# Kernel optimization log

Hardware: AMD Instinct MI355X
Metric: run time of the kernel (lower is better)

Reference implementation:

```python
import jax, jax.numpy as jnp
import numpy as np

N_NODES = 100000
N_EDGES = 1600000
H_DIM = 64  # pos(32) + vel(32)


def _mlp_init(key, d_in, d_hid, d_out):
    k1, k2 = jax.random.split(key)
    s1 = 1.0 / np.sqrt(d_in)
    s2 = 1.0 / np.sqrt(d_hid)
    w1 = jax.random.uniform(k1, (d_in, d_hid), jnp.float32, -s1, s1)
    w2 = jax.random.uniform(k2, (d_hid, d_out), jnp.float32, -s2, s2)
    return w1, jnp.zeros((d_hid,), jnp.float32), w2, jnp.zeros((d_out,), jnp.float32)


def setup_inputs() -> dict:
    key = jax.random.key(0)
    ks = jax.random.split(key, 6)
    pos = jax.random.normal(ks[0], (N_NODES, 32), jnp.float32)
    vel = jax.random.normal(ks[1], (N_NODES, 32), jnp.float32)
    edge_index = jax.random.randint(ks[2], (2, N_EDGES), 0, N_NODES, jnp.int32)
    msg_w1, msg_b1, msg_w2, msg_b2 = _mlp_init(ks[3], 2 * H_DIM, 64, 64)
    upd_w1, upd_b1, upd_w2, upd_b2 = _mlp_init(ks[4], H_DIM + 64, 64, 64)
    sp = 1.0 / np.sqrt(64)
    pred_w = jax.random.uniform(ks[5], (64, 32), jnp.float32, -sp, sp)
    pred_b = jnp.zeros((32,), jnp.float32)
    return dict(pos=pos, vel=vel, edge_index=edge_index,
                msg_w1=msg_w1, msg_b1=msg_b1, msg_w2=msg_w2, msg_b2=msg_b2,
                upd_w1=upd_w1, upd_b1=upd_b1, upd_w2=upd_w2, upd_b2=upd_b2,
                pred_w=pred_w, pred_b=pred_b)


def reference(pos, vel, edge_index,
              msg_w1, msg_b1, msg_w2, msg_b2,
              upd_w1, upd_b1, upd_w2, upd_b2,
              pred_w, pred_b):
    n = pos.shape[0]
    h = jnp.concatenate([pos, vel], axis=-1)              # [N, 64]
    src, dst = edge_index[0], edge_index[1]
    h_i = h[dst]                                          # [E, 64] target nodes
    h_j = h[src]                                          # [E, 64] source nodes
    # message MLP on concat(h_i, h_j)
    m = jnp.concatenate([h_i, h_j], axis=-1)              # [E, 128]
    m = jax.nn.relu(m @ msg_w1 + msg_b1) @ msg_w2 + msg_b2  # [E, 64]
    # scatter-add aggregate to target nodes
    aggr = jax.ops.segment_sum(m, dst, num_segments=n)    # [N, 64]
    # update MLP on concat(h, aggr)
    u = jnp.concatenate([h, aggr], axis=-1)               # [N, 128]
    u = jax.nn.relu(u @ upd_w1 + upd_b1) @ upd_w2 + upd_b2  # [N, 64]
    # linear prediction head -> acceleration
    return u @ pred_w + pred_b                            # [N, 32]
```

## Files before the change

kernel.cpp:

```cpp
#include <hip/hip_runtime.h>

#define NN 100000
#define NE 1600000
#define SB   391
#define NBKT 391
#define EPB  4096

typedef _Float16 f16x8 __attribute__((ext_vector_type(8)));
typedef float    f32x4 __attribute__((ext_vector_type(4)));

#define ZB   1563
#define PHB  3125
#define PWB  13

extern "C" __global__ void __launch_bounds__(256)
prep_kernel(const float* __restrict__ pos, const float* __restrict__ vel,
            const float* __restrict__ mw1, const float* __restrict__ mw2,
            const float* __restrict__ uw1, const float* __restrict__ uw2,
            const float* __restrict__ pw,
            _Float16* __restrict__ hh,
            _Float16* __restrict__ mw1f, _Float16* __restrict__ mw2f,
            _Float16* __restrict__ uw1f, _Float16* __restrict__ uw2f,
            _Float16* __restrict__ pwf,
            float* __restrict__ aggr)
{
    const int b = blockIdx.x, tid = threadIdx.x;
    if (b < ZB) {
        float4* p = (float4*)aggr;
        const int base4 = b * 1024 + tid;
        const float4 z = make_float4(0.f, 0.f, 0.f, 0.f);
#pragma unroll
        for (int k = 0; k < 4; ++k) {
            const int idx = base4 + k * 256;
            if (idx < NN * 16) p[idx] = z;
        }
    } else if (b < ZB + PHB) {
        const int t = (b - ZB) * 256 + tid;
        const int node = t >> 3, seg = t & 7;
        const float* src = (seg < 4) ? pos + (size_t)node * 32 + seg * 8
                                     : vel + (size_t)node * 32 + (seg - 4) * 8;
        const float4 a = ((const float4*)src)[0];
        const float4 c = ((const float4*)src)[1];
        f16x8 r;
        r[0]=(_Float16)a.x; r[1]=(_Float16)a.y; r[2]=(_Float16)a.z; r[3]=(_Float16)a.w;
        r[4]=(_Float16)c.x; r[5]=(_Float16)c.y; r[6]=(_Float16)c.z; r[7]=(_Float16)c.w;
        *(f16x8*)(hh + (size_t)node * 64 + seg * 8) = r;
    } else {
        const int t2 = (b - ZB - PHB) * 256 + tid;
        if (t2 < 1024) {
            const int t = t2 >> 8, kk = (t2 >> 6) & 3, l = t2 & 63;
            f16x8 r;
#pragma unroll
            for (int j = 0; j < 8; ++j)
                r[j] = (_Float16)mw1[(kk * 32 + (l >> 4) * 8 + j) * 64 + t * 16 + (l & 15)];
            *(f16x8*)(mw1f + (size_t)t2 * 8) = r;
        } else if (t2 < 1536) {
            const int i = t2 - 1024;
            const int t = i >> 7, kk = (i >> 6) & 1, l = i & 63;
            f16x8 r;
#pragma unroll
            for (int j = 0; j < 8; ++j)
                r[j] = (_Float16)mw2[(kk * 32 + (l >> 4) * 8 + j) * 64 + t * 16 + (l & 15)];
            *(f16x8*)(mw2f + (size_t)i * 8) = r;
        } else if (t2 < 2560) {
            const int i = t2 - 1536;
            const int t = i >> 8, kk = (i >> 6) & 3, l = i & 63;
            f16x8 r;
#pragma unroll
            for (int j = 0; j < 8; ++j)
                r[j] = (_Float16)uw1[(kk * 32 + (l >> 4) * 8 + j) * 64 + t * 16 + (l & 15)];
            *(f16x8*)(uw1f + (size_t)i * 8) = r;
        } else if (t2 < 3072) {
            const int i = t2 - 2560;
            const int t = i >> 7, kk = (i >> 6) & 1, l = i & 63;
            f16x8 r;
#pragma unroll
            for (int j = 0; j < 8; ++j)
                r[j] = (_Float16)uw2[(kk * 32 + (l >> 4) * 8 + j) * 64 + t * 16 + (l & 15)];
            *(f16x8*)(uw2f + (size_t)i * 8) = r;
        } else if (t2 < 3328) {
            const int i = t2 - 3072;
            const int t = i >> 7, kk = (i >> 6) & 1, l = i & 63;
            f16x8 r;
#pragma unroll
            for (int j = 0; j < 8; ++j)
                r[j] = (_Float16)pw[(kk * 32 + (l >> 4) * 8 + j) * 32 + t * 16 + (l & 15)];
            *(f16x8*)(pwf + (size_t)i * 8) = r;
        }
    }
}

extern "C" __global__ void __launch_bounds__(256)
sortA_kernel(const int* __restrict__ ei, int* __restrict__ cntm)
{
    __shared__ int lh[NBKT];
    const int tid = threadIdx.x, blk = blockIdx.x;
    for (int i = tid; i < NBKT; i += 256) lh[i] = 0;
    __syncthreads();
    const int e0 = blk * EPB;
#pragma unroll
    for (int k = 0; k < EPB / 256; ++k) {
        const int e = e0 + k * 256 + tid;
        if (e < NE) atomicAdd(&lh[ei[NE + e] >> 8], 1);
    }
    __syncthreads();
    for (int i = tid; i < NBKT; i += 256) cntm[blk * NBKT + i] = lh[i];
}

extern "C" __global__ void __launch_bounds__(512)
scancol_kernel(const int* __restrict__ cntm, int* __restrict__ offs,
               int* __restrict__ btot)
{
    __shared__ int s[512];
    const int tid = threadIdx.x, bkt = blockIdx.x;
    const int v = (tid < SB) ? cntm[tid * NBKT + bkt] : 0;
    s[tid] = v;
    __syncthreads();
    for (int off = 1; off < 512; off <<= 1) {
        int t = (tid >= off) ? s[tid - off] : 0;
        __syncthreads();
        s[tid] += t;
        __syncthreads();
    }
    if (tid < SB) offs[tid * NBKT + bkt] = s[tid] - v;
    if (tid == SB - 1) btot[bkt] = s[tid];
}

extern "C" __global__ void __launch_bounds__(512)
scanb_kernel(const int* __restrict__ btot, int* __restrict__ bbase)
{
    __shared__ int s[512];
    const int tid = threadIdx.x;
    const int v = (tid < NBKT) ? btot[tid] : 0;
    s[tid] = v;
    __syncthreads();
    for (int off = 1; off < 512; off <<= 1) {
        int t = (tid >= off) ? s[tid - off] : 0;
        __syncthreads();
        s[tid] += t;
        __syncthreads();
    }
    if (tid < NBKT) bbase[tid] = s[tid] - v;
    if (tid == NBKT - 1) bbase[NBKT] = s[tid];
}

extern "C" __global__ void __launch_bounds__(256)
sortC_kernel(const int* __restrict__ ei, const int* __restrict__ offs,
             const int* __restrict__ bbase, int2* __restrict__ sd_tmp)
{
    __shared__ int lh[NBKT];
    __shared__ int lo[NBKT];
    const int tid = threadIdx.x, blk = blockIdx.x;
    for (int i = tid; i < NBKT; i += 256) {
        lh[i] = 0;
        lo[i] = bbase[i] + offs[blk * NBKT + i];
    }
    __syncthreads();
    const int e0 = blk * EPB;
#pragma unroll
    for (int k = 0; k < EPB / 256; ++k) {
        const int e = e0 + k * 256 + tid;
        if (e < NE) {
            const int s = ei[e], d = ei[NE + e];
            const int bkt = d >> 8;
            const int r = atomicAdd(&lh[bkt], 1);
            sd_tmp[lo[bkt] + r] = make_int2(s, d);
        }
    }
}

extern "C" __global__ void __launch_bounds__(256)
sortD_kernel(const int2* __restrict__ sd_tmp, const int* __restrict__ bbase,
             int2* __restrict__ sd2)
{
    __shared__ int h[256];
    __shared__ int s[256];
    __shared__ int dbase[256];
    const int tid = threadIdx.x, bkt = blockIdx.x;
    const int s0 = bbase[bkt], s1 = bbase[bkt + 1];
    const int n = s1 - s0;
    h[tid] = 0;
    __syncthreads();
    for (int k = tid; k < n; k += 256)
        atomicAdd(&h[sd_tmp[s0 + k].y & 255], 1);
    __syncthreads();
    const int v = h[tid];
    s[tid] = v;
    __syncthreads();
    for (int off = 1; off < 256; off <<= 1) {
        int t = (tid >= off) ? s[tid - off] : 0;
        __syncthreads();
        s[tid] += t;
        __syncthreads();
    }
    dbase[tid] = s[tid] - v;
    __syncthreads();
    h[tid] = 0;
    __syncthreads();
    for (int k = tid; k < n; k += 256) {
        const int2 e = sd_tmp[s0 + k];
        const int dl = e.y & 255;
        const int r = atomicAdd(&h[dl], 1);
        sd2[s0 + dbase[dl] + r] = e;
    }
}

extern "C" __global__ void __launch_bounds__(256)
edgeagg_kernel(const _Float16* __restrict__ hh,
               const int2* __restrict__ sd,
               const _Float16* __restrict__ w1f, const _Float16* __restrict__ w2f,
               const float* __restrict__ b1, const float* __restrict__ b2,
               float* __restrict__ aggr)
{
    __shared__ _Float16 sW1[4 * 4 * 64 * 8];
    __shared__ _Float16 sW2[4 * 2 * 64 * 8];
    __shared__ _Float16 sT[4][16 * 64];

    const int tid = threadIdx.x;
    const int wave = tid >> 6, lane = tid & 63;
    const int m = lane & 15, g = lane >> 4;
    const int wslot = (blockIdx.x * 4 + wave) * 64;

    const int2 sdv = sd[wslot + lane];

    const int prevd = __shfl_up(sdv.y, 1, 64);
    const unsigned long long bmask = __ballot(lane == 0 || sdv.y != prevd);

    {
        const uint4* g1 = (const uint4*)w1f; uint4* s1 = (uint4*)sW1;
#pragma unroll
        for (int i = 0; i < 4; ++i) s1[i * 256 + tid] = g1[i * 256 + tid];
        const uint4* g2 = (const uint4*)w2f; uint4* s2 = (uint4*)sW2;
#pragma unroll
        for (int i = 0; i < 2; ++i) s2[i * 256 + tid] = g2[i * 256 + tid];
    }

    const float bb1[4] = { b1[m], b1[16 + m], b1[32 + m], b1[48 + m] };
    const float bb2[4] = { b2[m], b2[16 + m], b2[32 + m], b2[48 + m] };

    __syncthreads();

    _Float16* Y = sT[wave];

    float racc = 0.0f;
    int   rnode = __builtin_amdgcn_readlane(sdv.y, 0);
    int   firstRun = 1;

    f16x8 Abuf[2][4];
    {
        const int ns = __shfl(sdv.x, m, 64);
        const int nd = __shfl(sdv.y, m, 64);
        const _Float16* hd = hh + (size_t)nd * 64 + g * 8;
        const _Float16* hs = hh + (size_t)ns * 64 + g * 8;
        Abuf[0][0] = *(const f16x8*)(hd);
        Abuf[0][1] = *(const f16x8*)(hd + 32);
        Abuf[0][2] = *(const f16x8*)(hs);
        Abuf[0][3] = *(const f16x8*)(hs + 32);
    }

#pragma unroll
    for (int it = 0; it < 4; ++it) {
        const int cur = it & 1;
        if (it < 3) {
            const int ns = __shfl(sdv.x, (it + 1) * 16 + m, 64);
            const int nd = __shfl(sdv.y, (it + 1) * 16 + m, 64);
            const _Float16* hd = hh + (size_t)nd * 64 + g * 8;
            const _Float16* hs = hh + (size_t)ns * 64 + g * 8;
            Abuf[cur ^ 1][0] = *(const f16x8*)(hd);
            Abuf[cur ^ 1][1] = *(const f16x8*)(hd + 32);
            Abuf[cur ^ 1][2] = *(const f16x8*)(hs);
            Abuf[cur ^ 1][3] = *(const f16x8*)(hs + 32);
        }

        f32x4 acc[4] = {};
#pragma unroll
        for (int t = 0; t < 4; ++t) {
#pragma unroll
            for (int kk = 0; kk < 4; ++kk) {
                const f16x8 b = *(const f16x8*)(sW1 + ((t * 4 + kk) * 64 + lane) * 8);
                acc[t] = __builtin_amdgcn_mfma_f32_16x16x32_f16(Abuf[cur][kk], b, acc[t], 0, 0, 0);
            }
        }

#pragma unroll
        for (int t = 0; t < 4; ++t) {
#pragma unroll
            for (int r = 0; r < 4; ++r) {
                const float y = fmaxf(acc[t][r] + bb1[t], 0.0f);
                const int row = g * 4 + r, col = t * 16 + m;
                const int byteoff = row * 128 + ((2 * col) ^ ((row & 7) << 4));
                *(_Float16*)((char*)Y + byteoff) = (_Float16)y;
            }
        }
        asm volatile("s_waitcnt lgkmcnt(0)" ::: "memory");
        __builtin_amdgcn_sched_barrier(0);

        f16x8 a2[2];
#pragma unroll
        for (int kk = 0; kk < 2; ++kk) {
            const int c = kk * 4 + g;
            a2[kk] = *(const f16x8*)((char*)Y + m * 128 + ((c * 16) ^ ((m & 7) << 4)));
        }
        asm volatile("s_waitcnt lgkmcnt(0)" ::: "memory");
        __builtin_amdgcn_sched_barrier(0);

        f32x4 acc2[4] = {};
#pragma unroll
        for (int kk = 0; kk < 2; ++kk) {
#pragma unroll
            for (int t = 0; t < 4; ++t) {
                const f16x8 b = *(const f16x8*)(sW2 + ((t * 2 + kk) * 64 + lane) * 8);
                acc2[t] = __builtin_amdgcn_mfma_f32_16x16x32_f16(a2[kk], b, acc2[t], 0, 0, 0);
            }
        }
#pragma unroll
        for (int t = 0; t < 4; ++t)
#pragma unroll
            for (int r = 0; r < 4; ++r) acc2[t][r] += bb2[t];

        const unsigned tm = (unsigned)((bmask >> (it * 16)) & 0xFFFFull) | 0x10000u;
        int a = 0;
        while (a < 16) {
            const int b = a + 1 + __builtin_ctz(tm >> (a + 1));
            const int d = __builtin_amdgcn_readlane(sdv.y, it * 16 + a);
            if (d != rnode) {
                float* ap = aggr + (size_t)rnode * 64 + lane;
                if (firstRun) atomicAdd(ap, racc);
                else          *ap = racc;
                firstRun = 0; racc = 0.0f; rnode = d;
            }
            float p0 = 0.f, p1 = 0.f, p2 = 0.f, p3 = 0.f;
#pragma unroll
            for (int r = 0; r < 4; ++r) {
                const int rowl = 4 * g + r;
                const bool in = (rowl >= a) && (rowl < b);
                p0 += in ? acc2[0][r] : 0.f;
                p1 += in ? acc2[1][r] : 0.f;
                p2 += in ? acc2[2][r] : 0.f;
                p3 += in ? acc2[3][r] : 0.f;
            }
            p0 += __shfl_xor(p0, 16); p0 += __shfl_xor(p0, 32);
            p1 += __shfl_xor(p1, 16); p1 += __shfl_xor(p1, 32);
            p2 += __shfl_xor(p2, 16); p2 += __shfl_xor(p2, 32);
            p3 += __shfl_xor(p3, 16); p3 += __shfl_xor(p3, 32);
            const float v = (g == 0) ? p0 : (g == 1) ? p1 : (g == 2) ? p2 : p3;
            racc += v;
            a = b;
        }
    }
    atomicAdd(aggr + (size_t)rnode * 64 + lane, racc);
}

extern "C" __global__ void __launch_bounds__(256)
node_mfma_kernel(const _Float16* __restrict__ hh, const float* __restrict__ aggr,
                 const _Float16* __restrict__ uw1f, const _Float16* __restrict__ uw2f,
                 const _Float16* __restrict__ pwf,
                 const float* __restrict__ b1, const float* __restrict__ b2,
                 const float* __restrict__ pb, float* __restrict__ out)
{
    __shared__ _Float16 sU1[4 * 4 * 64 * 8];
    __shared__ _Float16 sU2[4 * 2 * 64 * 8];
    __shared__ _Float16 sPW[2 * 2 * 64 * 8];
    __shared__ _Float16 sT[4][16 * 64];

    const int tid = threadIdx.x;
    {
        const uint4* g1 = (const uint4*)uw1f; uint4* s1 = (uint4*)sU1;
#pragma unroll
        for (int i = 0; i < 4; ++i) s1[i * 256 + tid] = g1[i * 256 + tid];
        const uint4* g2 = (const uint4*)uw2f; uint4* s2 = (uint4*)sU2;
#pragma unroll
        for (int i = 0; i < 2; ++i) s2[i * 256 + tid] = g2[i * 256 + tid];
        const uint4* g3 = (const uint4*)pwf;  uint4* s3 = (uint4*)sPW;
        s3[tid] = g3[tid];
    }
    __syncthreads();

    const int wave = tid >> 6, lane = tid & 63;
    const int m = lane & 15, g = lane >> 4;
    const int nb = (blockIdx.x * 4 + wave) * 16;
    const int v = nb + m;
    const int vl = (v < NN) ? v : (NN - 1);

    const _Float16* hv = hh + (size_t)vl * 64 + g * 8;
    const f16x8 a0 = *(const f16x8*)(hv);
    const f16x8 a1 = *(const f16x8*)(hv + 32);
    const float* av = aggr + (size_t)vl * 64 + g * 8;
    const float4 x0 = *(const float4*)(av),      x1 = *(const float4*)(av + 4);
    const float4 y0 = *(const float4*)(av + 32), y1 = *(const float4*)(av + 36);
    f16x8 a2, a3;
    a2[0]=(_Float16)x0.x; a2[1]=(_Float16)x0.y; a2[2]=(_Float16)x0.z; a2[3]=(_Float16)x0.w;
    a2[4]=(_Float16)x1.x; a2[5]=(_Float16)x1.y; a2[6]=(_Float16)x1.z; a2[7]=(_Float16)x1.w;
    a3[0]=(_Float16)y0.x; a3[1]=(_Float16)y0.y; a3[2]=(_Float16)y0.z; a3[3]=(_Float16)y0.w;
    a3[4]=(_Float16)y1.x; a3[5]=(_Float16)y1.y; a3[6]=(_Float16)y1.z; a3[7]=(_Float16)y1.w;

    f32x4 acc[4] = {};
#pragma unroll
    for (int t = 0; t < 4; ++t) {
        acc[t] = __builtin_amdgcn_mfma_f32_16x16x32_f16(
            a0, *(const f16x8*)(sU1 + ((t * 4 + 0) * 64 + lane) * 8), acc[t], 0, 0, 0);
        acc[t] = __builtin_amdgcn_mfma_f32_16x16x32_f16(
            a1, *(const f16x8*)(sU1 + ((t * 4 + 1) * 64 + lane) * 8), acc[t], 0, 0, 0);
        acc[t] = __builtin_amdgcn_mfma_f32_16x16x32_f16(
            a2, *(const f16x8*)(sU1 + ((t * 4 + 2) * 64 + lane) * 8), acc[t], 0, 0, 0);
        acc[t] = __builtin_amdgcn_mfma_f32_16x16x32_f16(
            a3, *(const f16x8*)(sU1 + ((t * 4 + 3) * 64 + lane) * 8), acc[t], 0, 0, 0);
    }

    _Float16* Y = sT[wave];
#pragma unroll
    for (int t = 0; t < 4; ++t) {
        const float bb = b1[t * 16 + m];
#pragma unroll
        for (int r = 0; r < 4; ++r) {
            const float y = fmaxf(acc[t][r] + bb, 0.0f);
            const int row = g * 4 + r, col = t * 16 + m;
            const int byteoff = row * 128 + ((2 * col) ^ ((row & 7) << 4));
            *(_Float16*)((char*)Y + byteoff) = (_Float16)y;
        }
    }
    asm volatile("s_waitcnt lgkmcnt(0)" ::: "memory");
    __builtin_amdgcn_sched_barrier(0);

    f16x8 ay[2];
#pragma unroll
    for (int kk = 0; kk < 2; ++kk) {
        const int c = kk * 4 + g;
        ay[kk] = *(const f16x8*)((char*)Y + m * 128 + ((c * 16) ^ ((m & 7) << 4)));
    }
    asm volatile("s_waitcnt lgkmcnt(0)" ::: "memory");
    __builtin_amdgcn_sched_barrier(0);

    f32x4 acc2[4] = {};
#pragma unroll
    for (int kk = 0; kk < 2; ++kk) {
#pragma unroll
        for (int t = 0; t < 4; ++t) {
            const f16x8 b = *(const f16x8*)(sU2 + ((t * 2 + kk) * 64 + lane) * 8);
            acc2[t] = __builtin_amdgcn_mfma_f32_16x16x32_f16(ay[kk], b, acc2[t], 0, 0, 0);
        }
    }

#pragma unroll
    for (int t = 0; t < 4; ++t) {
        const float bb = b2[t * 16 + m];
#pragma unroll
        for (int r = 0; r < 4; ++r) {
            const float u = acc2[t][r] + bb;
            const int row = g * 4 + r, col = t * 16 + m;
            const int byteoff = row * 128 + ((2 * col) ^ ((row & 7) << 4));
            *(_Float16*)((char*)Y + byteoff) = (_Float16)u;
        }
    }
    asm volatile("s_waitcnt lgkmcnt(0)" ::: "memory");
    __builtin_amdgcn_sched_barrier(0);

    f16x8 au[2];
#pragma unroll
    for (int kk = 0; kk < 2; ++kk) {
        const int c = kk * 4 + g;
        au[kk] = *(const f16x8*)((char*)Y + m * 128 + ((c * 16) ^ ((m & 7) << 4)));
    }
    asm volatile("s_waitcnt lgkmcnt(0)" ::: "memory");
    __builtin_amdgcn_sched_barrier(0);

    f32x4 acc3[2] = {};
#pragma unroll
    for (int kk = 0; kk < 2; ++kk) {
#pragma unroll
        for (int t = 0; t < 2; ++t) {
            const f16x8 b = *(const f16x8*)(sPW + ((t * 2 + kk) * 64 + lane) * 8);
            acc3[t] = __builtin_amdgcn_mfma_f32_16x16x32_f16(au[kk], b, acc3[t], 0, 0, 0);
        }
    }

    float* F = (float*)Y;
#pragma unroll
    for (int t = 0; t < 2; ++t) {
        const float bb = pb[t * 16 + m];
#pragma unroll
        for (int r = 0; r < 4; ++r) {
            const int row = g * 4 + r, col = t * 16 + m;
            const int byteoff = row * 128 + ((4 * col) ^ ((row & 7) << 4));
            *(float*)((char*)F + byteoff) = acc3[t][r] + bb;
        }
    }
    asm volatile("s_waitcnt lgkmcnt(0)" ::: "memory");
    __builtin_amdgcn_sched_barrier(0);

    const int row = lane >> 2, q = lane & 3;
    const float4 o0 = *(const float4*)((char*)F + row * 128 + ((q * 16)       ^ ((row & 7) << 4)));
    const float4 o1 = *(const float4*)((char*)F + row * 128 + (((q + 4) * 16) ^ ((row & 7) << 4)));
    if (nb + row < NN) {
        float4* op = (float4*)(out + (size_t)(nb + row) * 32);
        op[q]     = o0;
        op[q + 4] = o1;
    }
}

extern "C" __global__ void __launch_bounds__(256)
edge_msg_kernel(const float* __restrict__ pos, const float* __restrict__ vel,
                const int* __restrict__ ei,
                const float* __restrict__ w1, const float* __restrict__ b1,
                const float* __restrict__ w2, const float* __restrict__ b2,
                float* __restrict__ aggr)
{
    const int e = blockIdx.x * 256 + threadIdx.x;
    if (e >= NE) return;
    const int ns = ei[e];
    const int nd = ei[NE + e];
    float y[64];
#pragma unroll
    for (int j = 0; j < 64; ++j) y[j] = b1[j];
    for (int part = 0; part < 4; ++part) {
        const int    node  = (part < 2) ? nd : ns;
        const float* basep = (part & 1) ? vel : pos;
        const float4* xp = reinterpret_cast<const float4*>(basep + (size_t)node * 32);
        const float*  wp = w1 + part * 32 * 64;
        for (int q = 0; q < 8; ++q) {
            const float4 xv = xp[q];
#pragma unroll
            for (int kk = 0; kk < 4; ++kk) {
                const float xs = (kk == 0) ? xv.x : (kk == 1) ? xv.y
                               : (kk == 2) ? xv.z : xv.w;
                const float* wr = wp + (q * 4 + kk) * 64;
#pragma unroll
                for (int j = 0; j < 64; ++j) y[j] = fmaf(xs, wr[j], y[j]);
            }
        }
    }
    float mm[64];
#pragma unroll
    for (int c = 0; c < 64; ++c) mm[c] = b2[c];
#pragma unroll
    for (int j = 0; j < 64; ++j) {
        const float yj = fmaxf(y[j], 0.0f);
        const float* wr = w2 + j * 64;
#pragma unroll
        for (int c = 0; c < 64; ++c) mm[c] = fmaf(yj, wr[c], mm[c]);
    }
    float* ap = aggr + (size_t)nd * 64;
#pragma unroll
    for (int c = 0; c < 64; ++c) atomicAdd(ap + c, mm[c]);
}

extern "C" __global__ void __launch_bounds__(256)
node_upd_kernel(const float* __restrict__ pos, const float* __restrict__ vel,
                const float* __restrict__ aggr,
                const float* __restrict__ w1, const float* __restrict__ b1,
                const float* __restrict__ w2, const float* __restrict__ b2,
                const float* __restrict__ pw, const float* __restrict__ pb,
                float* __restrict__ out)
{
    const int v = blockIdx.x * 256 + threadIdx.x;
    if (v >= NN) return;

    float y[64];
#pragma unroll
    for (int j = 0; j < 64; ++j) y[j] = b1[j];
    for (int part = 0; part < 4; ++part) {
        const float* basep = (part == 0) ? pos + (size_t)v * 32
                           : (part == 1) ? vel + (size_t)v * 32
                           : aggr + (size_t)v * 64 + (size_t)(part - 2) * 32;
        const float4* xp = reinterpret_cast<const float4*>(basep);
        const float*  wp = w1 + part * 32 * 64;
        for (int q = 0; q < 8; ++q) {
            const float4 xv = xp[q];
#pragma unroll
            for (int kk = 0; kk < 4; ++kk) {
                const float xs = (kk == 0) ? xv.x : (kk == 1) ? xv.y
                               : (kk == 2) ? xv.z : xv.w;
                const float* wr = wp + (q * 4 + kk) * 64;
#pragma unroll
                for (int j = 0; j < 64; ++j) y[j] = fmaf(xs, wr[j], y[j]);
            }
        }
    }

    float u[64];
#pragma unroll
    for (int c = 0; c < 64; ++c) u[c] = b2[c];
#pragma unroll
    for (int j = 0; j < 64; ++j) {
        const float yj = fmaxf(y[j], 0.0f);
        const float* wr = w2 + j * 64;
#pragma unroll
        for (int c = 0; c < 64; ++c) u[c] = fmaf(yj, wr[c], u[c]);
    }

    float o[32];
#pragma unroll
    for (int c = 0; c < 32; ++c) o[c] = pb[c];
#pragma unroll
    for (int j = 0; j < 64; ++j) {
        const float* wr = pw + j * 32;
#pragma unroll
        for (int c = 0; c < 32; ++c) o[c] = fmaf(u[j], wr[c], o[c]);
    }

    float4* op = reinterpret_cast<float4*>(out + (size_t)v * 32);
#pragma unroll
    for (int q = 0; q < 8; ++q)
        op[q] = make_float4(o[q * 4], o[q * 4 + 1], o[q * 4 + 2], o[q * 4 + 3]);
}

extern "C" void kernel_launch(void* const* d_in, const int* in_sizes, int n_in,
                              void* d_out, int out_size, void* d_ws, size_t ws_size,
                              hipStream_t stream)
{
    const float* pos = (const float*)d_in[0];
    const float* vel = (const float*)d_in[1];
    const int*   ei  = (const int*)d_in[2];
    const float* mw1 = (const float*)d_in[3];
    const float* mb1 = (const float*)d_in[4];
    const float* mw2 = (const float*)d_in[5];
    const float* mb2 = (const float*)d_in[6];
    const float* uw1 = (const float*)d_in[7];
    const float* ub1 = (const float*)d_in[8];
    const float* uw2 = (const float*)d_in[9];
    const float* ub2 = (const float*)d_in[10];
    const float* pw  = (const float*)d_in[11];
    const float* pb  = (const float*)d_in[12];
    float* out = (float*)d_out;

    char* ws = (char*)d_ws;
    size_t off = 0;
    float*    aggr   = (float*)(ws + off);    off += (size_t)NN * 64 * 4;
    _Float16* hh     = (_Float16*)(ws + off); off += (size_t)NN * 64 * 2;
    int2*     sd_tmp = (int2*)(ws + off);     off += (size_t)NE * 8;
    int2*     sd2    = (int2*)(ws + off);     off += (size_t)NE * 8;
    int*      cntm   = (int*)(ws + off);      off += (size_t)SB * NBKT * 4;
    int*      offs   = (int*)(ws + off);      off += (size_t)SB * NBKT * 4;
    int*      btot   = (int*)(ws + off);      off += 512 * 4;
    int*      bbase  = (int*)(ws + off);      off += 512 * 4;
    _Float16* mw1f   = (_Float16*)(ws + off); off += 1024 * 8 * 2;
    _Float16* mw2f   = (_Float16*)(ws + off); off += 512 * 8 * 2;
    _Float16* uw1f   = (_Float16*)(ws + off); off += 1024 * 8 * 2;
    _Float16* uw2f   = (_Float16*)(ws + off); off += 512 * 8 * 2;
    _Float16* pwf    = (_Float16*)(ws + off); off += 256 * 8 * 2;
    const size_t need_full = off;

    if (ws_size >= need_full) {
        prep_kernel<<<ZB + PHB + PWB, 256, 0, stream>>>(
            pos, vel, mw1, mw2, uw1, uw2, pw,
            hh, mw1f, mw2f, uw1f, uw2f, pwf, aggr);
        sortA_kernel<<<SB, 256, 0, stream>>>(ei, cntm);
        scancol_kernel<<<NBKT, 512, 0, stream>>>(cntm, offs, btot);
        scanb_kernel<<<1, 512, 0, stream>>>(btot, bbase);
        sortC_kernel<<<SB, 256, 0, stream>>>(ei, offs, bbase, sd_tmp);
        sortD_kernel<<<NBKT, 256, 0, stream>>>(sd_tmp, bbase, sd2);
        edgeagg_kernel<<<NE / 256, 256, 0, stream>>>(
            hh, sd2, mw1f, mw2f, mb1, mb2, aggr);
        node_mfma_kernel<<<(NN + 63) / 64, 256, 0, stream>>>(
            hh, aggr, uw1f, uw2f, pwf, ub1, ub2, pb, out);
    } else {
        float* aggr2 = (float*)d_ws;
        hipMemsetAsync(aggr2, 0, (size_t)NN * 64 * sizeof(float), stream);
        edge_msg_kernel<<<NE / 256, 256, 0, stream>>>(pos, vel, ei,
                                                      mw1, mb1, mw2, mb2, aggr2);
        node_upd_kernel<<<(NN + 255) / 256, 256, 0, stream>>>(
            pos, vel, aggr2, uw1, ub1, uw2, ub2, pw, pb, out);
    }
}
```

Baseline: 138.7 us.

## Fuse sort histogram into prep kernel, widen edge blocks, add fast no-boundary path

```diff
diff --git a/kernel.cpp b/kernel.cpp
--- a/kernel.cpp
+++ b/kernel.cpp
@@ -15,6 +15,7 @@
 
 extern "C" __global__ void __launch_bounds__(256)
 prep_kernel(const float* __restrict__ pos, const float* __restrict__ vel,
+            const int* __restrict__ ei,
             const float* __restrict__ mw1, const float* __restrict__ mw2,
             const float* __restrict__ uw1, const float* __restrict__ uw2,
             const float* __restrict__ pw,
@@ -22,8 +23,9 @@
             _Float16* __restrict__ mw1f, _Float16* __restrict__ mw2f,
             _Float16* __restrict__ uw1f, _Float16* __restrict__ uw2f,
             _Float16* __restrict__ pwf,
-            float* __restrict__ aggr)
-{
+            float* __restrict__ aggr, int* __restrict__ cntm)
+{
+    __shared__ int lh[NBKT];
     const int b = blockIdx.x, tid = threadIdx.x;
     if (b < ZB) {
         float4* p = (float4*)aggr;
@@ -45,7 +47,7 @@
         r[0]=(_Float16)a.x; r[1]=(_Float16)a.y; r[2]=(_Float16)a.z; r[3]=(_Float16)a.w;
         r[4]=(_Float16)c.x; r[5]=(_Float16)c.y; r[6]=(_Float16)c.z; r[7]=(_Float16)c.w;
         *(f16x8*)(hh + (size_t)node * 64 + seg * 8) = r;
-    } else {
+    } else if (b < ZB + PHB + PWB) {
         const int t2 = (b - ZB - PHB) * 256 + tid;
         if (t2 < 1024) {
             const int t = t2 >> 8, kk = (t2 >> 6) & 3, l = t2 & 63;
@@ -87,24 +89,19 @@
                 r[j] = (_Float16)pw[(kk * 32 + (l >> 4) * 8 + j) * 32 + t * 16 + (l & 15)];
             *(f16x8*)(pwf + (size_t)i * 8) = r;
         }
-    }
-}
-
-extern "C" __global__ void __launch_bounds__(256)
-sortA_kernel(const int* __restrict__ ei, int* __restrict__ cntm)
-{
-    __shared__ int lh[NBKT];
-    const int tid = threadIdx.x, blk = blockIdx.x;
-    for (int i = tid; i < NBKT; i += 256) lh[i] = 0;
-    __syncthreads();
-    const int e0 = blk * EPB;
-#pragma unroll
-    for (int k = 0; k < EPB / 256; ++k) {
-        const int e = e0 + k * 256 + tid;
-        if (e < NE) atomicAdd(&lh[ei[NE + e] >> 8], 1);
-    }
-    __syncthreads();
-    for (int i = tid; i < NBKT; i += 256) cntm[blk * NBKT + i] = lh[i];
+    } else {
+        const int blk = b - (ZB + PHB + PWB);
+        for (int i = tid; i < NBKT; i += 256) lh[i] = 0;
+        __syncthreads();
+        const int e0 = blk * EPB;
+#pragma unroll
+        for (int k = 0; k < EPB / 256; ++k) {
+            const int e = e0 + k * 256 + tid;
+            if (e < NE) atomicAdd(&lh[ei[NE + e] >> 8], 1);
+        }
+        __syncthreads();
+        for (int i = tid; i < NBKT; i += 256) cntm[blk * NBKT + i] = lh[i];
+    }
 }
 
 extern "C" __global__ void __launch_bounds__(512)
@@ -205,7 +202,7 @@
     }
 }
 
-extern "C" __global__ void __launch_bounds__(256)
+extern "C" __global__ void __launch_bounds__(512, 8)
 edgeagg_kernel(const _Float16* __restrict__ hh,
                const int2* __restrict__ sd,
                const _Float16* __restrict__ w1f, const _Float16* __restrict__ w2f,
@@ -214,12 +211,12 @@
 {
     __shared__ _Float16 sW1[4 * 4 * 64 * 8];
     __shared__ _Float16 sW2[4 * 2 * 64 * 8];
-    __shared__ _Float16 sT[4][16 * 64];
+    __shared__ _Float16 sT[8][16 * 64];
 
     const int tid = threadIdx.x;
     const int wave = tid >> 6, lane = tid & 63;
     const int m = lane & 15, g = lane >> 4;
-    const int wslot = (blockIdx.x * 4 + wave) * 64;
+    const int wslot = (blockIdx.x * 8 + wave) * 64;
 
     const int2 sdv = sd[wslot + lane];
 
@@ -229,10 +226,9 @@
     {
         const uint4* g1 = (const uint4*)w1f; uint4* s1 = (uint4*)sW1;
 #pragma unroll
-        for (int i = 0; i < 4; ++i) s1[i * 256 + tid] = g1[i * 256 + tid];
+        for (int i = 0; i < 2; ++i) s1[i * 512 + tid] = g1[i * 512 + tid];
         const uint4* g2 = (const uint4*)w2f; uint4* s2 = (uint4*)sW2;
-#pragma unroll
-        for (int i = 0; i < 2; ++i) s2[i * 256 + tid] = g2[i * 256 + tid];
+        s2[tid] = g2[tid];
     }
 
     const float bb1[4] = { b1[m], b1[16 + m], b1[32 + m], b1[48 + m] };
@@ -319,33 +315,46 @@
             for (int r = 0; r < 4; ++r) acc2[t][r] += bb2[t];
 
         const unsigned tm = (unsigned)((bmask >> (it * 16)) & 0xFFFFull) | 0x10000u;
-        int a = 0;
-        while (a < 16) {
-            const int b = a + 1 + __builtin_ctz(tm >> (a + 1));
-            const int d = __builtin_amdgcn_readlane(sdv.y, it * 16 + a);
-            if (d != rnode) {
-                float* ap = aggr + (size_t)rnode * 64 + lane;
-                if (firstRun) atomicAdd(ap, racc);
-                else          *ap = racc;
-                firstRun = 0; racc = 0.0f; rnode = d;
-            }
+        if (tm == 0x10000u) {
             float p0 = 0.f, p1 = 0.f, p2 = 0.f, p3 = 0.f;
 #pragma unroll
             for (int r = 0; r < 4; ++r) {
-                const int rowl = 4 * g + r;
-                const bool in = (rowl >= a) && (rowl < b);
-                p0 += in ? acc2[0][r] : 0.f;
-                p1 += in ? acc2[1][r] : 0.f;
-                p2 += in ? acc2[2][r] : 0.f;
-                p3 += in ? acc2[3][r] : 0.f;
+                p0 += acc2[0][r]; p1 += acc2[1][r];
+                p2 += acc2[2][r]; p3 += acc2[3][r];
             }
             p0 += __shfl_xor(p0, 16); p0 += __shfl_xor(p0, 32);
             p1 += __shfl_xor(p1, 16); p1 += __shfl_xor(p1, 32);
             p2 += __shfl_xor(p2, 16); p2 += __shfl_xor(p2, 32);
             p3 += __shfl_xor(p3, 16); p3 += __shfl_xor(p3, 32);
-            const float v = (g == 0) ? p0 : (g == 1) ? p1 : (g == 2) ? p2 : p3;
-            racc += v;
-            a = b;
+            racc += (g == 0) ? p0 : (g == 1) ? p1 : (g == 2) ? p2 : p3;
+        } else {
+            int a = 0;
+            while (a < 16) {
+                const int b = a + 1 + __builtin_ctz(tm >> (a + 1));
+                const int d = __builtin_amdgcn_readlane(sdv.y, it * 16 + a);
+                if (d != rnode) {
+                    float* ap = aggr + (size_t)rnode * 64 + lane;
+                    if (firstRun) atomicAdd(ap, racc);
+                    else          *ap = racc;
+                    firstRun = 0; racc = 0.0f; rnode = d;
+                }
+                float p0 = 0.f, p1 = 0.f, p2 = 0.f, p3 = 0.f;
+#pragma unroll
+                for (int r = 0; r < 4; ++r) {
+                    const int rowl = 4 * g + r;
+                    const bool in = (rowl >= a) && (rowl < b);
+                    p0 += in ? acc2[0][r] : 0.f;
+                    p1 += in ? acc2[1][r] : 0.f;
+                    p2 += in ? acc2[2][r] : 0.f;
+                    p3 += in ? acc2[3][r] : 0.f;
+                }
+                p0 += __shfl_xor(p0, 16); p0 += __shfl_xor(p0, 32);
+                p1 += __shfl_xor(p1, 16); p1 += __shfl_xor(p1, 32);
+                p2 += __shfl_xor(p2, 16); p2 += __shfl_xor(p2, 32);
+                p3 += __shfl_xor(p3, 16); p3 += __shfl_xor(p3, 32);
+                racc += (g == 0) ? p0 : (g == 1) ? p1 : (g == 2) ? p2 : p3;
+                a = b;
+            }
         }
     }
     atomicAdd(aggr + (size_t)rnode * 64 + lane, racc);
@@ -641,15 +650,14 @@
     const size_t need_full = off;
 
     if (ws_size >= need_full) {
-        prep_kernel<<<ZB + PHB + PWB, 256, 0, stream>>>(
-            pos, vel, mw1, mw2, uw1, uw2, pw,
-            hh, mw1f, mw2f, uw1f, uw2f, pwf, aggr);
-        sortA_kernel<<<SB, 256, 0, stream>>>(ei, cntm);
+        prep_kernel<<<ZB + PHB + PWB + SB, 256, 0, stream>>>(
+            pos, vel, ei, mw1, mw2, uw1, uw2, pw,
+            hh, mw1f, mw2f, uw1f, uw2f, pwf, aggr, cntm);
         scancol_kernel<<<NBKT, 512, 0, stream>>>(cntm, offs, btot);
         scanb_kernel<<<1, 512, 0, stream>>>(btot, bbase);
         sortC_kernel<<<SB, 256, 0, stream>>>(ei, offs, bbase, sd_tmp);
         sortD_kernel<<<NBKT, 256, 0, stream>>>(sd_tmp, bbase, sd2);
-        edgeagg_kernel<<<NE / 256, 256, 0, stream>>>(
+        edgeagg_kernel<<<NE / 512, 512, 0, stream>>>(
             hh, sd2, mw1f, mw2f, mb1, mb2, aggr);
         node_mfma_kernel<<<(NN + 63) / 64, 256, 0, stream>>>(
             hh, aggr, uw1f, uw2f, pwf, ub1, ub2, pb, out);
```

Measured after the change: 217.5 us. +56.8%, slower.
